# Kernel optimization log

Hardware: AMD Instinct MI355X
Metric: run time of the kernel (lower is better)

## Reference

```python
import jax, jax.numpy as jnp
import numpy as np

BN_EPS = 1e-5


def setup_inputs() -> dict:
    key = jax.random.key(0)
    ks = jax.random.split(key, 4)
    B, C, N = 4, 256, 4096
    Cq = C // 4
    return {
        "input_embedding": jax.random.normal(ks[0], (B, C, N), dtype=jnp.float32),
        "w_qk": jax.random.normal(ks[1], (Cq, C), dtype=jnp.float32) * (1.0 / np.sqrt(C)),
        "w_v": jax.random.normal(ks[2], (C, C), dtype=jnp.float32) * (1.0 / np.sqrt(C)),
        "b_v": jnp.zeros((C,), dtype=jnp.float32),
        "w_trans": jax.random.normal(ks[3], (C, C), dtype=jnp.float32) * (1.0 / np.sqrt(C)),
        "b_trans": jnp.zeros((C,), dtype=jnp.float32),
        "bn_gamma": jnp.ones((C,), dtype=jnp.float32),
        "bn_beta": jnp.zeros((C,), dtype=jnp.float32),
        "bn_mean": jnp.zeros((C,), dtype=jnp.float32),
        "bn_var": jnp.ones((C,), dtype=jnp.float32),
    }


def reference(input_embedding, w_qk, w_v, b_v, w_trans, b_trans,
              bn_gamma, bn_beta, bn_mean, bn_var):
    x = input_embedding  # (B, C, N)
    # 1x1 conv1d == channel matmul. Q and K share the same weight (tied in __init__).
    Q = jnp.einsum("qc,bcn->bnq", w_qk, x)              # (B, N, C/4)
    K = jnp.einsum("qc,bcn->bqn", w_qk, x)              # (B, C/4, N)
    V = jnp.einsum("oc,bcn->bon", w_v, x) + b_v[None, :, None]  # (B, C, N)
    scores = jnp.einsum("bnq,bqm->bnm", Q, K)           # (B, N, N)
    attn = jax.nn.softmax(scores, axis=-1)              # row softmax (dim=-1)
    # column L1 renormalization (sum over dim=1)
    attn = attn / (1e-9 + jnp.sum(attn, axis=1, keepdims=True))
    new_features = jnp.einsum("bcn,bnm->bcm", V, attn)  # (B, C, N)
    # offset residual -> trans conv -> BN (inference form) -> ReLU
    y = jnp.einsum("oc,bcn->bon", w_trans, x - new_features) + b_trans[None, :, None]
    inv_std = jax.lax.rsqrt(bn_var + BN_EPS)
    y = (y - bn_mean[None, :, None]) * (bn_gamma * inv_std)[None, :, None] + bn_beta[None, :, None]
    return jax.nn.relu(y)
```

## Files before the change

kernel.cpp:

```cpp
#include <hip/hip_runtime.h>

#define BATCH 4
#define CCH 256
#define NN 4096
#define CQ 64

typedef __bf16 bf16;
typedef __bf16 bf16x4 __attribute__((ext_vector_type(4)));
typedef __bf16 bf16x8 __attribute__((ext_vector_type(8)));
typedef float f32x4 __attribute__((ext_vector_type(4)));

static __device__ __forceinline__ f32x4 mfma16(bf16x8 a, bf16x8 b, f32x4 c) {
  return __builtin_amdgcn_mfma_f32_16x16x32_bf16(a, b, c, 0, 0, 0);
}

__global__ __launch_bounds__(256) void prep_kernel(const float* __restrict__ w_qk,
                                                   const float* __restrict__ w_v,
                                                   const float* __restrict__ w_trans,
                                                   bf16* __restrict__ wkvb,
                                                   bf16* __restrict__ wtb) {
  int i = blockIdx.x * 256 + threadIdx.x;
  if (i < 320 * 256) {
    int r = i >> 8, c = i & 255;
    float v = (r < 64) ? w_qk[r * 256 + c] : w_v[(r - 64) * 256 + c];
    wkvb[i] = (bf16)v;
  }
  if (i < 256 * 256) wtb[i] = (bf16)w_trans[i];
}

__global__ __launch_bounds__(256) void transpose_kernel(const float* __restrict__ x,
                                                        bf16* __restrict__ xTb) {
  __shared__ float t[64][65];
  int b = blockIdx.z, c0 = blockIdx.y * 64, n0 = blockIdx.x * 64;
  int tx = threadIdx.x & 63, ty = threadIdx.x >> 6;
  const float* xp = x + ((size_t)b * CCH + c0) * NN + n0;
#pragma unroll
  for (int j = 0; j < 16; ++j) {
    int cl = ty * 16 + j;
    t[tx][cl] = xp[(size_t)cl * NN + tx];
  }
  __syncthreads();
  bf16* op = xTb + ((size_t)b * NN + n0) * CCH + c0;
#pragma unroll
  for (int j = 0; j < 16; ++j) {
    int nl = ty * 16 + j;
    op[(size_t)nl * CCH + tx] = (bf16)t[nl][tx];
  }
}

__global__ __launch_bounds__(256) void kv_kernel(const bf16* __restrict__ wkvb,
                                                 const bf16* __restrict__ xTb,
                                                 const float* __restrict__ b_v,
                                                 bf16* __restrict__ Knq,
                                                 bf16* __restrict__ V,
                                                 float* __restrict__ sq) {
  int b = blockIdx.z, chunk = blockIdx.y;
  int w = threadIdx.x >> 6, lane = threadIdx.x & 63, lg = lane >> 4, lr = lane & 15;
  int n0 = blockIdx.x * 256 + w * 64;
  int r0 = chunk * 64;
  f32x4 z = {0.f, 0.f, 0.f, 0.f};
  f32x4 acc[4][4];
#pragma unroll
  for (int i = 0; i < 4; ++i)
#pragma unroll
    for (int j = 0; j < 4; ++j) acc[i][j] = z;

  for (int ks = 0; ks < 8; ++ks) {
    bf16x8 af[4], bb[4];
#pragma unroll
    for (int t = 0; t < 4; ++t)
      af[t] = *(const bf16x8*)(wkvb + (size_t)(r0 + 16 * t + lr) * 256 + 32 * ks + 8 * lg);
#pragma unroll
    for (int t = 0; t < 4; ++t)
      bb[t] = *(const bf16x8*)(xTb + ((size_t)b * NN + n0 + 16 * t + lr) * CCH + 32 * ks + 8 * lg);
#pragma unroll
    for (int tc = 0; tc < 4; ++tc)
#pragma unroll
      for (int tn = 0; tn < 4; ++tn) acc[tc][tn] = mfma16(af[tc], bb[tn], acc[tc][tn]);
  }

  if (chunk == 0) {
    float sqn[4];
#pragma unroll
    for (int tn = 0; tn < 4; ++tn) {
      int n = n0 + 16 * tn + lr;
#pragma unroll
      for (int tc = 0; tc < 4; ++tc) {
        bf16x4 kb;
#pragma unroll
        for (int r = 0; r < 4; ++r) kb[r] = (bf16)acc[tc][tn][r];
        *(bf16x4*)(Knq + ((size_t)b * NN + n) * CQ + 16 * tc + lg * 4) = kb;
      }
      float s = 0.f;
#pragma unroll
      for (int tc = 0; tc < 4; ++tc)
#pragma unroll
        for (int r = 0; r < 4; ++r) s += acc[tc][tn][r] * acc[tc][tn][r];
      s += __shfl_xor(s, 16);
      s += __shfl_xor(s, 32);
      sqn[tn] = s;
    }
    if (lane < 16) {
#pragma unroll
      for (int tn = 0; tn < 4; ++tn)
        sq[(size_t)b * NN + n0 + 16 * tn + lane] = sqn[tn];
    }
  } else {
#pragma unroll
    for (int tc = 0; tc < 4; ++tc) {
      int c4 = (chunk - 1) * 64 + 16 * tc + lg * 4;
      f32x4 bv = *(const f32x4*)(b_v + c4);
#pragma unroll
      for (int tn = 0; tn < 4; ++tn) {
        int n = n0 + 16 * tn + lr;
#pragma unroll
        for (int r = 0; r < 4; ++r)
          V[((size_t)b * CCH + c4 + r) * NN + n] = (bf16)(acc[tc][tn][r] + bv[r]);
      }
    }
  }
}

__global__ __launch_bounds__(512) void rnorm_kernel(const bf16* __restrict__ Knq,
                                                    const float* __restrict__ sq,
                                                    float* __restrict__ invr) {
  __shared__ float lsl[8][16];
  int b = blockIdx.y, n0 = blockIdx.x * 64;
  int w = threadIdx.x >> 6, lane = threadIdx.x & 63, lg = lane >> 4, lr = lane & 15;
  int sn = w & 3, mh = w >> 2;
  const bf16* Kb = Knq + (size_t)b * NN * CQ;
  int nr = n0 + 16 * sn;
  bf16x8 a0 = *(const bf16x8*)(Kb + (size_t)(nr + lr) * CQ + 8 * lg);
  bf16x8 a1 = *(const bf16x8*)(Kb + (size_t)(nr + lr) * CQ + 32 + 8 * lg);
  f32x4 sh = *(const f32x4*)(sq + (size_t)b * NN + nr + lg * 4);
  f32x4 z = {0.f, 0.f, 0.f, 0.f};
  f32x4 ls = z;
  for (int mt = mh * (NN / 2); mt < (mh + 1) * (NN / 2); mt += 64) {
#pragma unroll
    for (int j = 0; j < 4; ++j) {
      int m0 = mt + 16 * j;
      bf16x8 b0 = *(const bf16x8*)(Kb + (size_t)(m0 + lr) * CQ + 8 * lg);
      bf16x8 b1 = *(const bf16x8*)(Kb + (size_t)(m0 + lr) * CQ + 32 + 8 * lg);
      f32x4 s = mfma16(a0, b0, z);
      s = mfma16(a1, b1, s);
#pragma unroll
      for (int r = 0; r < 4; ++r) ls[r] += __expf(s[r] - sh[r]);
    }
  }
#pragma unroll
  for (int d = 1; d < 16; d <<= 1)
#pragma unroll
    for (int r = 0; r < 4; ++r) ls[r] += __shfl_xor(ls[r], d);
  if (lr == 0) {
#pragma unroll
    for (int r = 0; r < 4; ++r) lsl[w][lg * 4 + r] = ls[r];
  }
  __syncthreads();
  if (threadIdx.x < 64) {
    int t = threadIdx.x;
    float S = lsl[t >> 4][t & 15] + lsl[(t >> 4) + 4][t & 15];
    invr[(size_t)b * NN + n0 + t] = 1.0f / S;
  }
}

#define SWZ(row, colb) ((colb) ^ (((row)&7) << 4))
__global__ __launch_bounds__(512) void pv_kernel(const bf16* __restrict__ Knq,
                                                 const bf16* __restrict__ V,
                                                 const float* __restrict__ sq,
                                                 const float* __restrict__ invr,
                                                 const bf16* __restrict__ xTb,
                                                 bf16* __restrict__ DTb) {
  __shared__ bf16 P2[2][64][128];
  __shared__ float csl[8][64];
  __shared__ float csv[64];
  int lin = blockIdx.y * (NN / 64) + blockIdx.x;
  int xcd = lin & 7, slot = lin >> 3;
  int b = xcd >> 1;
  int m0 = (((xcd & 1) << 5) | slot) * 64;
  int w = threadIdx.x >> 6, lane = threadIdx.x & 63, lg = lane >> 4, lr = lane & 15;
  const bf16* Kb = Knq + (size_t)b * NN * CQ;
  const bf16* Vb = V + (size_t)b * CCH * NN;
  f32x4 z = {0.f, 0.f, 0.f, 0.f};

  bf16x8 bS[4][2];
#pragma unroll
  for (int tj = 0; tj < 4; ++tj) {
    bS[tj][0] = *(const bf16x8*)(Kb + (size_t)(m0 + 16 * tj + lr) * CQ + 8 * lg);
    bS[tj][1] = *(const bf16x8*)(Kb + (size_t)(m0 + 16 * tj + lr) * CQ + 32 + 8 * lg);
  }

  f32x4 acc[2][4];
#pragma unroll
  for (int i = 0; i < 2; ++i)
#pragma unroll
    for (int j = 0; j < 4; ++j) acc[i][j] = z;
  float cs[4] = {0.f, 0.f, 0.f, 0.f};

#define S_PHASE(STEP, BUF)                                                          \
  {                                                                                 \
    int nr_ = (STEP) * 128 + 16 * w;                                                \
    bf16x8 a0_ = *(const bf16x8*)(Kb + (size_t)(nr_ + lr) * CQ + 8 * lg);           \
    bf16x8 a1_ = *(const bf16x8*)(Kb + (size_t)(nr_ + lr) * CQ + 32 + 8 * lg);      \
    f32x4 sh_ = *(const f32x4*)(sq + (size_t)b * NN + nr_ + lg * 4);                \
    f32x4 ri_ = *(const f32x4*)(invr + (size_t)b * NN + nr_ + lg * 4);              \
    _Pragma("unroll") for (int tj = 0; tj < 4; ++tj) {                              \
      f32x4 s4 = mfma16(a0_, bS[tj][0], z);                                         \
      s4 = mfma16(a1_, bS[tj][1], s4);                                              \
      bf16x4 pb;                                                                    \
      _Pragma("unroll") for (int r = 0; r < 4; ++r) {                               \
        float p_ = __expf(s4[r] - sh_[r]) * ri_[r];                                 \
        cs[tj] += p_;                                                               \
        pb[r] = (bf16)p_;                                                           \
      }                                                                             \
      *(bf16x4*)((char*)&P2[BUF][16 * tj + lr][0] + SWZ(lr, 2 * (16 * w + 4 * lg))) = pb; \
    }                                                                               \
  }

  S_PHASE(0, 0);
  __syncthreads();

  for (int s = 0; s < NN / 128; ++s) {
    int cur = s & 1;
    int ns = s * 128;
    bf16x8 bp[4][4];
#pragma unroll
    for (int ks = 0; ks < 4; ++ks)
#pragma unroll
      for (int tj = 0; tj < 4; ++tj)
        bp[ks][tj] = *(const bf16x8*)((char*)&P2[cur][16 * tj + lr][0] +
                                      SWZ(16 * tj + lr, 2 * (32 * ks + 8 * lg)));
    bf16x8 av[4][2];
#pragma unroll
    for (int ks = 0; ks < 4; ++ks)
#pragma unroll
      for (int tc = 0; tc < 2; ++tc)
        av[ks][tc] = *(const bf16x8*)(Vb + (size_t)(32 * w + 16 * tc + lr) * NN + ns + 32 * ks + 8 * lg);
    if (s + 1 < NN / 128) S_PHASE(s + 1, cur ^ 1);
#pragma unroll
    for (int ks = 0; ks < 4; ++ks)
#pragma unroll
      for (int tc = 0; tc < 2; ++tc)
#pragma unroll
        for (int tj = 0; tj < 4; ++tj) acc[tc][tj] = mfma16(av[ks][tc], bp[ks][tj], acc[tc][tj]);
    __syncthreads();
  }

#pragma unroll
  for (int tj = 0; tj < 4; ++tj) {
    cs[tj] += __shfl_xor(cs[tj], 16);
    cs[tj] += __shfl_xor(cs[tj], 32);
  }
  if (lane < 16) {
#pragma unroll
    for (int tj = 0; tj < 4; ++tj) csl[w][16 * tj + lane] = cs[tj];
  }
  __syncthreads();
  if (threadIdx.x < 64) {
    int t = threadIdx.x;
    float s = 0.f;
#pragma unroll
    for (int ww = 0; ww < 8; ++ww) s += csl[ww][t];
    csv[t] = 1.0f / (1e-9f + s);
  }
  __syncthreads();

#pragma unroll
  for (int tj = 0; tj < 4; ++tj) {
    int ml = 16 * tj + lr;
    int m = m0 + ml;
    float ci = csv[ml];
#pragma unroll
    for (int tc = 0; tc < 2; ++tc) {
      int c4 = 32 * w + 16 * tc + lg * 4;
      bf16x4 xv = *(const bf16x4*)(xTb + ((size_t)b * NN + m) * CCH + c4);
      bf16x4 dv;
#pragma unroll
      for (int r = 0; r < 4; ++r) dv[r] = (bf16)((float)xv[r] - acc[tc][tj][r] * ci);
      *(bf16x4*)(DTb + ((size_t)b * NN + m) * CCH + c4) = dv;
    }
  }
}

__global__ __launch_bounds__(256) void final_kernel(const bf16* __restrict__ wtb,
                                                    const bf16* __restrict__ DTb,
                                                    const float* __restrict__ b_trans,
                                                    const float* __restrict__ gamma,
                                                    const float* __restrict__ beta,
                                                    const float* __restrict__ mean,
                                                    const float* __restrict__ var,
                                                    float* __restrict__ out) {
  int b = blockIdx.y;
  int w = threadIdx.x >> 6, lane = threadIdx.x & 63, lg = lane >> 4, lr = lane & 15;
  int n0 = blockIdx.x * 64;
  f32x4 z = {0.f, 0.f, 0.f, 0.f};
  f32x4 acc[4][4];
#pragma unroll
  for (int i = 0; i < 4; ++i)
#pragma unroll
    for (int j = 0; j < 4; ++j) acc[i][j] = z;

  for (int ks = 0; ks < 8; ++ks) {
    bf16x8 a[4], bb[4];
#pragma unroll
    for (int t = 0; t < 4; ++t)
      a[t] = *(const bf16x8*)(wtb + (size_t)(64 * w + 16 * t + lr) * 256 + 32 * ks + 8 * lg);
#pragma unroll
    for (int t = 0; t < 4; ++t)
      bb[t] = *(const bf16x8*)(DTb + ((size_t)b * NN + n0 + 16 * t + lr) * CCH + 32 * ks + 8 * lg);
#pragma unroll
    for (int tc = 0; tc < 4; ++tc)
#pragma unroll
      for (int tn = 0; tn < 4; ++tn) acc[tc][tn] = mfma16(a[tc], bb[tn], acc[tc][tn]);
  }

#pragma unroll
  for (int tc = 0; tc < 4; ++tc) {
    int c4 = 64 * w + 16 * tc + lg * 4;
    f32x4 bt = *(const f32x4*)(b_trans + c4);
    f32x4 gm = *(const f32x4*)(gamma + c4);
    f32x4 be = *(const f32x4*)(beta + c4);
    f32x4 mn = *(const f32x4*)(mean + c4);
    f32x4 vr = *(const f32x4*)(var + c4);
    f32x4 sc, shv;
#pragma unroll
    for (int r = 0; r < 4; ++r) {
      sc[r] = gm[r] * rsqrtf(vr[r] + 1e-5f);
      shv[r] = be[r] - mn[r] * sc[r];
    }
#pragma unroll
    for (int tn = 0; tn < 4; ++tn) {
      int n = n0 + 16 * tn + lr;
#pragma unroll
      for (int r = 0; r < 4; ++r) {
        float y = (acc[tc][tn][r] + bt[r]) * sc[r] + shv[r];
        out[((size_t)b * CCH + c4 + r) * NN + n] = fmaxf(y, 0.0f);
      }
    }
  }
}

extern "C" void kernel_launch(void* const* d_in, const int* in_sizes, int n_in,
                              void* d_out, int out_size, void* d_ws, size_t ws_size,
                              hipStream_t stream) {
  const float* x = (const float*)d_in[0];
  const float* w_qk = (const float*)d_in[1];
  const float* w_v = (const float*)d_in[2];
  const float* b_v = (const float*)d_in[3];
  const float* w_trans = (const float*)d_in[4];
  const float* b_trans = (const float*)d_in[5];
  const float* gamma = (const float*)d_in[6];
  const float* beta = (const float*)d_in[7];
  const float* mean = (const float*)d_in[8];
  const float* var = (const float*)d_in[9];
  float* out = (float*)d_out;

  char* p = (char*)d_ws;
  bf16* wkvb = (bf16*)p; p += (size_t)320 * 256 * 2;
  bf16* wtb = (bf16*)p;  p += (size_t)256 * 256 * 2;
  bf16* xTb = (bf16*)p;  p += (size_t)BATCH * NN * CCH * 2;
  bf16* Knq = (bf16*)p;  p += (size_t)BATCH * NN * CQ * 2;
  bf16* V = (bf16*)p;    p += (size_t)BATCH * CCH * NN * 2;
  float* sq = (float*)p;   p += (size_t)BATCH * NN * 4;
  float* invr = (float*)p; p += (size_t)BATCH * NN * 4;
  bf16* DTb = (bf16*)p;  p += (size_t)BATCH * NN * CCH * 2;

  hipLaunchKernelGGL(prep_kernel, dim3(320), dim3(256), 0, stream, w_qk, w_v, w_trans, wkvb, wtb);
  hipLaunchKernelGGL(transpose_kernel, dim3(NN / 64, CCH / 64, BATCH), dim3(256), 0, stream, x, xTb);
  hipLaunchKernelGGL(kv_kernel, dim3(NN / 256, 5, BATCH), dim3(256), 0, stream, wkvb, xTb, b_v, Knq, V, sq);
  hipLaunchKernelGGL(rnorm_kernel, dim3(NN / 64, BATCH), dim3(512), 0, stream, Knq, sq, invr);
  hipLaunchKernelGGL(pv_kernel, dim3(NN / 64, BATCH), dim3(512), 0, stream, Knq, V, sq, invr, xTb, DTb);
  hipLaunchKernelGGL(final_kernel, dim3(NN / 64, BATCH), dim3(256), 0, stream, wtb, DTb, b_trans, gamma, beta, mean, var, out);
}
```

Measured before the change: 287.6 us.

## Halve column tiles per block to double grid size across attention kernels

Every kernel now handles 32 columns per block instead of 64 (kv handles 128 instead of 256), so each launch has twice as many blocks. rnorm and pv drop from 512 to 256 threads with launch_bounds(256,2). Inside pv, each wave now owns 64 output channels and two 16-row score groups instead of 32 channels, which changes the work split and reuse inside the block. The aim is better CU occupancy and load balance on a wide GPU, at the cost of reading V from global memory twice as often per output column and doing more redundant K loads.

```diff
diff --git a/kernel.cpp b/kernel.cpp
--- a/kernel.cpp
+++ b/kernel.cpp
@@ -56,33 +56,34 @@
                                                  float* __restrict__ sq) {
   int b = blockIdx.z, chunk = blockIdx.y;
   int w = threadIdx.x >> 6, lane = threadIdx.x & 63, lg = lane >> 4, lr = lane & 15;
-  int n0 = blockIdx.x * 256 + w * 64;
+  int n0 = blockIdx.x * 128 + w * 32;
   int r0 = chunk * 64;
   f32x4 z = {0.f, 0.f, 0.f, 0.f};
-  f32x4 acc[4][4];
+  f32x4 acc[4][2];
 #pragma unroll
   for (int i = 0; i < 4; ++i)
 #pragma unroll
-    for (int j = 0; j < 4; ++j) acc[i][j] = z;
-
+    for (int j = 0; j < 2; ++j) acc[i][j] = z;
+
+#pragma unroll
   for (int ks = 0; ks < 8; ++ks) {
-    bf16x8 af[4], bb[4];
+    bf16x8 af[4], bb[2];
 #pragma unroll
     for (int t = 0; t < 4; ++t)
       af[t] = *(const bf16x8*)(wkvb + (size_t)(r0 + 16 * t + lr) * 256 + 32 * ks + 8 * lg);
 #pragma unroll
-    for (int t = 0; t < 4; ++t)
+    for (int t = 0; t < 2; ++t)
       bb[t] = *(const bf16x8*)(xTb + ((size_t)b * NN + n0 + 16 * t + lr) * CCH + 32 * ks + 8 * lg);
 #pragma unroll
     for (int tc = 0; tc < 4; ++tc)
 #pragma unroll
-      for (int tn = 0; tn < 4; ++tn) acc[tc][tn] = mfma16(af[tc], bb[tn], acc[tc][tn]);
+      for (int tn = 0; tn < 2; ++tn) acc[tc][tn] = mfma16(af[tc], bb[tn], acc[tc][tn]);
   }
 
   if (chunk == 0) {
-    float sqn[4];
-#pragma unroll
-    for (int tn = 0; tn < 4; ++tn) {
+    float sqn[2];
+#pragma unroll
+    for (int tn = 0; tn < 2; ++tn) {
       int n = n0 + 16 * tn + lr;
 #pragma unroll
       for (int tc = 0; tc < 4; ++tc) {
@@ -102,7 +103,7 @@
     }
     if (lane < 16) {
 #pragma unroll
-      for (int tn = 0; tn < 4; ++tn)
+      for (int tn = 0; tn < 2; ++tn)
         sq[(size_t)b * NN + n0 + 16 * tn + lane] = sqn[tn];
     }
   } else {
@@ -111,7 +112,7 @@
       int c4 = (chunk - 1) * 64 + 16 * tc + lg * 4;
       f32x4 bv = *(const f32x4*)(b_v + c4);
 #pragma unroll
-      for (int tn = 0; tn < 4; ++tn) {
+      for (int tn = 0; tn < 2; ++tn) {
         int n = n0 + 16 * tn + lr;
 #pragma unroll
         for (int r = 0; r < 4; ++r)
@@ -121,99 +122,113 @@
   }
 }
 
-__global__ __launch_bounds__(512) void rnorm_kernel(const bf16* __restrict__ Knq,
-                                                    const float* __restrict__ sq,
-                                                    float* __restrict__ invr) {
-  __shared__ float lsl[8][16];
-  int b = blockIdx.y, n0 = blockIdx.x * 64;
+__global__ __launch_bounds__(256, 2) void rnorm_kernel(const bf16* __restrict__ Knq,
+                                                       const float* __restrict__ sq,
+                                                       float* __restrict__ invr) {
+  __shared__ float lsl[4][2][16];
+  int b = blockIdx.y, n0 = blockIdx.x * 32;
   int w = threadIdx.x >> 6, lane = threadIdx.x & 63, lg = lane >> 4, lr = lane & 15;
-  int sn = w & 3, mh = w >> 2;
   const bf16* Kb = Knq + (size_t)b * NN * CQ;
-  int nr = n0 + 16 * sn;
-  bf16x8 a0 = *(const bf16x8*)(Kb + (size_t)(nr + lr) * CQ + 8 * lg);
-  bf16x8 a1 = *(const bf16x8*)(Kb + (size_t)(nr + lr) * CQ + 32 + 8 * lg);
-  f32x4 sh = *(const f32x4*)(sq + (size_t)b * NN + nr + lg * 4);
+  bf16x8 a0[2], a1[2];
+  f32x4 sh[2];
+#pragma unroll
+  for (int g = 0; g < 2; ++g) {
+    int nr = n0 + 16 * g;
+    a0[g] = *(const bf16x8*)(Kb + (size_t)(nr + lr) * CQ + 8 * lg);
+    a1[g] = *(const bf16x8*)(Kb + (size_t)(nr + lr) * CQ + 32 + 8 * lg);
+    sh[g] = *(const f32x4*)(sq + (size_t)b * NN + nr + lg * 4);
+  }
   f32x4 z = {0.f, 0.f, 0.f, 0.f};
-  f32x4 ls = z;
-  for (int mt = mh * (NN / 2); mt < (mh + 1) * (NN / 2); mt += 64) {
+  f32x4 ls[2] = {z, z};
+  for (int mt = w * (NN / 4); mt < (w + 1) * (NN / 4); mt += 64) {
 #pragma unroll
     for (int j = 0; j < 4; ++j) {
       int m0 = mt + 16 * j;
       bf16x8 b0 = *(const bf16x8*)(Kb + (size_t)(m0 + lr) * CQ + 8 * lg);
       bf16x8 b1 = *(const bf16x8*)(Kb + (size_t)(m0 + lr) * CQ + 32 + 8 * lg);
-      f32x4 s = mfma16(a0, b0, z);
-      s = mfma16(a1, b1, s);
-#pragma unroll
-      for (int r = 0; r < 4; ++r) ls[r] += __expf(s[r] - sh[r]);
+#pragma unroll
+      for (int g = 0; g < 2; ++g) {
+        f32x4 s = mfma16(a0[g], b0, z);
+        s = mfma16(a1[g], b1, s);
+#pragma unroll
+        for (int r = 0; r < 4; ++r) ls[g][r] += __expf(s[r] - sh[g][r]);
+      }
     }
   }
 #pragma unroll
   for (int d = 1; d < 16; d <<= 1)
 #pragma unroll
-    for (int r = 0; r < 4; ++r) ls[r] += __shfl_xor(ls[r], d);
+    for (int g = 0; g < 2; ++g)
+#pragma unroll
+      for (int r = 0; r < 4; ++r) ls[g][r] += __shfl_xor(ls[g][r], d);
   if (lr == 0) {
 #pragma unroll
-    for (int r = 0; r < 4; ++r) lsl[w][lg * 4 + r] = ls[r];
-  }
-  __syncthreads();
-  if (threadIdx.x < 64) {
-    int t = threadIdx.x;
-    float S = lsl[t >> 4][t & 15] + lsl[(t >> 4) + 4][t & 15];
-    invr[(size_t)b * NN + n0 + t] = 1.0f / S;
+    for (int g = 0; g < 2; ++g)
+#pragma unroll
+      for (int r = 0; r < 4; ++r) lsl[w][g][lg * 4 + r] = ls[g][r];
+  }
+  __syncthreads();
+  if (threadIdx.x < 32) {
+    int g = threadIdx.x >> 4, i = threadIdx.x & 15;
+    float S = lsl[0][g][i] + lsl[1][g][i] + lsl[2][g][i] + lsl[3][g][i];
+    invr[(size_t)b * NN + n0 + 16 * g + i] = 1.0f / S;
   }
 }
 
 #define SWZ(row, colb) ((colb) ^ (((row)&7) << 4))
-__global__ __launch_bounds__(512) void pv_kernel(const bf16* __restrict__ Knq,
-                                                 const bf16* __restrict__ V,
-                                                 const float* __restrict__ sq,
-                                                 const float* __restrict__ invr,
-                                                 const bf16* __restrict__ xTb,
-                                                 bf16* __restrict__ DTb) {
-  __shared__ bf16 P2[2][64][128];
-  __shared__ float csl[8][64];
-  __shared__ float csv[64];
-  int lin = blockIdx.y * (NN / 64) + blockIdx.x;
+__global__ __launch_bounds__(256, 2) void pv_kernel(const bf16* __restrict__ Knq,
+                                                    const bf16* __restrict__ V,
+                                                    const float* __restrict__ sq,
+                                                    const float* __restrict__ invr,
+                                                    const bf16* __restrict__ xTb,
+                                                    bf16* __restrict__ DTb) {
+  __shared__ bf16 P2[2][32][128];
+  __shared__ float csl[4][32];
+  __shared__ float csv[32];
+  int lin = blockIdx.y * (NN / 32) + blockIdx.x;
   int xcd = lin & 7, slot = lin >> 3;
   int b = xcd >> 1;
-  int m0 = (((xcd & 1) << 5) | slot) * 64;
+  int m0 = (((xcd & 1) << 6) | slot) * 32;
   int w = threadIdx.x >> 6, lane = threadIdx.x & 63, lg = lane >> 4, lr = lane & 15;
   const bf16* Kb = Knq + (size_t)b * NN * CQ;
   const bf16* Vb = V + (size_t)b * CCH * NN;
   f32x4 z = {0.f, 0.f, 0.f, 0.f};
 
-  bf16x8 bS[4][2];
-#pragma unroll
-  for (int tj = 0; tj < 4; ++tj) {
+  bf16x8 bS[2][2];
+#pragma unroll
+  for (int tj = 0; tj < 2; ++tj) {
     bS[tj][0] = *(const bf16x8*)(Kb + (size_t)(m0 + 16 * tj + lr) * CQ + 8 * lg);
     bS[tj][1] = *(const bf16x8*)(Kb + (size_t)(m0 + 16 * tj + lr) * CQ + 32 + 8 * lg);
   }
 
-  f32x4 acc[2][4];
-#pragma unroll
-  for (int i = 0; i < 2; ++i)
-#pragma unroll
-    for (int j = 0; j < 4; ++j) acc[i][j] = z;
-  float cs[4] = {0.f, 0.f, 0.f, 0.f};
-
-#define S_PHASE(STEP, BUF)                                                          \
-  {                                                                                 \
-    int nr_ = (STEP) * 128 + 16 * w;                                                \
-    bf16x8 a0_ = *(const bf16x8*)(Kb + (size_t)(nr_ + lr) * CQ + 8 * lg);           \
-    bf16x8 a1_ = *(const bf16x8*)(Kb + (size_t)(nr_ + lr) * CQ + 32 + 8 * lg);      \
-    f32x4 sh_ = *(const f32x4*)(sq + (size_t)b * NN + nr_ + lg * 4);                \
-    f32x4 ri_ = *(const f32x4*)(invr + (size_t)b * NN + nr_ + lg * 4);              \
-    _Pragma("unroll") for (int tj = 0; tj < 4; ++tj) {                              \
-      f32x4 s4 = mfma16(a0_, bS[tj][0], z);                                         \
-      s4 = mfma16(a1_, bS[tj][1], s4);                                              \
-      bf16x4 pb;                                                                    \
-      _Pragma("unroll") for (int r = 0; r < 4; ++r) {                               \
-        float p_ = __expf(s4[r] - sh_[r]) * ri_[r];                                 \
-        cs[tj] += p_;                                                               \
-        pb[r] = (bf16)p_;                                                           \
-      }                                                                             \
-      *(bf16x4*)((char*)&P2[BUF][16 * tj + lr][0] + SWZ(lr, 2 * (16 * w + 4 * lg))) = pb; \
-    }                                                                               \
+  f32x4 acc[4][2];
+#pragma unroll
+  for (int i = 0; i < 4; ++i)
+#pragma unroll
+    for (int j = 0; j < 2; ++j) acc[i][j] = z;
+  float cs[2] = {0.f, 0.f};
+
+#define S_PHASE(STEP, BUF)                                                            \
+  {                                                                                   \
+    _Pragma("unroll") for (int g = 0; g < 2; ++g) {                                   \
+      int nr_ = (STEP) * 128 + 32 * w + 16 * g;                                       \
+      bf16x8 a0_ = *(const bf16x8*)(Kb + (size_t)(nr_ + lr) * CQ + 8 * lg);           \
+      bf16x8 a1_ = *(const bf16x8*)(Kb + (size_t)(nr_ + lr) * CQ + 32 + 8 * lg);      \
+      f32x4 sh_ = *(const f32x4*)(sq + (size_t)b * NN + nr_ + lg * 4);                \
+      f32x4 ri_ = *(const f32x4*)(invr + (size_t)b * NN + nr_ + lg * 4);              \
+      _Pragma("unroll") for (int tj = 0; tj < 2; ++tj) {                              \
+        f32x4 s4 = mfma16(a0_, bS[tj][0], z);                                         \
+        s4 = mfma16(a1_, bS[tj][1], s4);                                              \
+        bf16x4 pb;                                                                    \
+        _Pragma("unroll") for (int r = 0; r < 4; ++r) {                               \
+          float p_ = __expf(s4[r] - sh_[r]) * ri_[r];                                 \
+          cs[tj] += p_;                                                               \
+          pb[r] = (bf16)p_;                                                           \
+        }                                                                             \
+        *(bf16x4*)((char*)&P2[BUF][16 * tj + lr][0] +                                 \
+                   SWZ(lr, 2 * (32 * w + 16 * g + 4 * lg))) = pb;                     \
+      }                                                                               \
+    }                                                                                 \
   }
 
   S_PHASE(0, 0);
@@ -222,56 +237,54 @@
   for (int s = 0; s < NN / 128; ++s) {
     int cur = s & 1;
     int ns = s * 128;
-    bf16x8 bp[4][4];
+    bf16x8 av[4][4];
 #pragma unroll
     for (int ks = 0; ks < 4; ++ks)
 #pragma unroll
-      for (int tj = 0; tj < 4; ++tj)
+      for (int tc = 0; tc < 4; ++tc)
+        av[ks][tc] = *(const bf16x8*)(Vb + (size_t)(64 * w + 16 * tc + lr) * NN + ns + 32 * ks + 8 * lg);
+    bf16x8 bp[4][2];
+#pragma unroll
+    for (int ks = 0; ks < 4; ++ks)
+#pragma unroll
+      for (int tj = 0; tj < 2; ++tj)
         bp[ks][tj] = *(const bf16x8*)((char*)&P2[cur][16 * tj + lr][0] +
                                       SWZ(16 * tj + lr, 2 * (32 * ks + 8 * lg)));
-    bf16x8 av[4][2];
+    if (s + 1 < NN / 128) S_PHASE(s + 1, cur ^ 1);
 #pragma unroll
     for (int ks = 0; ks < 4; ++ks)
 #pragma unroll
-      for (int tc = 0; tc < 2; ++tc)
-        av[ks][tc] = *(const bf16x8*)(Vb + (size_t)(32 * w + 16 * tc + lr) * NN + ns + 32 * ks + 8 * lg);
-    if (s + 1 < NN / 128) S_PHASE(s + 1, cur ^ 1);
-#pragma unroll
-    for (int ks = 0; ks < 4; ++ks)
-#pragma unroll
-      for (int tc = 0; tc < 2; ++tc)
-#pragma unroll
-        for (int tj = 0; tj < 4; ++tj) acc[tc][tj] = mfma16(av[ks][tc], bp[ks][tj], acc[tc][tj]);
+      for (int tc = 0; tc < 4; ++tc)
+#pragma unroll
+        for (int tj = 0; tj < 2; ++tj) acc[tc][tj] = mfma16(av[ks][tc], bp[ks][tj], acc[tc][tj]);
     __syncthreads();
   }
 
 #pragma unroll
-  for (int tj = 0; tj < 4; ++tj) {
+  for (int tj = 0; tj < 2; ++tj) {
     cs[tj] += __shfl_xor(cs[tj], 16);
     cs[tj] += __shfl_xor(cs[tj], 32);
   }
   if (lane < 16) {
 #pragma unroll
-    for (int tj = 0; tj < 4; ++tj) csl[w][16 * tj + lane] = cs[tj];
-  }
-  __syncthreads();
-  if (threadIdx.x < 64) {
+    for (int tj = 0; tj < 2; ++tj) csl[w][16 * tj + lane] = cs[tj];
+  }
+  __syncthreads();
+  if (threadIdx.x < 32) {
     int t = threadIdx.x;
-    float s = 0.f;
-#pragma unroll
-    for (int ww = 0; ww < 8; ++ww) s += csl[ww][t];
+    float s = csl[0][t] + csl[1][t] + csl[2][t] + csl[3][t];
     csv[t] = 1.0f / (1e-9f + s);
   }
   __syncthreads();
 
 #pragma unroll
-  for (int tj = 0; tj < 4; ++tj) {
+  for (int tj = 0; tj < 2; ++tj) {
     int ml = 16 * tj + lr;
     int m = m0 + ml;
     float ci = csv[ml];
 #pragma unroll
-    for (int tc = 0; tc < 2; ++tc) {
-      int c4 = 32 * w + 16 * tc + lg * 4;
+    for (int tc = 0; tc < 4; ++tc) {
+      int c4 = 64 * w + 16 * tc + lg * 4;
       bf16x4 xv = *(const bf16x4*)(xTb + ((size_t)b * NN + m) * CCH + c4);
       bf16x4 dv;
 #pragma unroll
@@ -291,26 +304,27 @@
                                                     float* __restrict__ out) {
   int b = blockIdx.y;
   int w = threadIdx.x >> 6, lane = threadIdx.x & 63, lg = lane >> 4, lr = lane & 15;
-  int n0 = blockIdx.x * 64;
+  int n0 = blockIdx.x * 32;
   f32x4 z = {0.f, 0.f, 0.f, 0.f};
-  f32x4 acc[4][4];
+  f32x4 acc[4][2];
 #pragma unroll
   for (int i = 0; i < 4; ++i)
 #pragma unroll
-    for (int j = 0; j < 4; ++j) acc[i][j] = z;
-
+    for (int j = 0; j < 2; ++j) acc[i][j] = z;
+
+#pragma unroll
   for (int ks = 0; ks < 8; ++ks) {
-    bf16x8 a[4], bb[4];
+    bf16x8 a[4], bb[2];
 #pragma unroll
     for (int t = 0; t < 4; ++t)
       a[t] = *(const bf16x8*)(wtb + (size_t)(64 * w + 16 * t + lr) * 256 + 32 * ks + 8 * lg);
 #pragma unroll
-    for (int t = 0; t < 4; ++t)
+    for (int t = 0; t < 2; ++t)
       bb[t] = *(const bf16x8*)(DTb + ((size_t)b * NN + n0 + 16 * t + lr) * CCH + 32 * ks + 8 * lg);
 #pragma unroll
     for (int tc = 0; tc < 4; ++tc)
 #pragma unroll
-      for (int tn = 0; tn < 4; ++tn) acc[tc][tn] = mfma16(a[tc], bb[tn], acc[tc][tn]);
+      for (int tn = 0; tn < 2; ++tn) acc[tc][tn] = mfma16(a[tc], bb[tn], acc[tc][tn]);
   }
 
 #pragma unroll
@@ -328,7 +342,7 @@
       shv[r] = be[r] - mn[r] * sc[r];
     }
 #pragma unroll
-    for (int tn = 0; tn < 4; ++tn) {
+    for (int tn = 0; tn < 2; ++tn) {
       int n = n0 + 16 * tn + lr;
 #pragma unroll
       for (int r = 0; r < 4; ++r) {
@@ -366,8 +380,8 @@
 
   hipLaunchKernelGGL(prep_kernel, dim3(320), dim3(256), 0, stream, w_qk, w_v, w_trans, wkvb, wtb);
   hipLaunchKernelGGL(transpose_kernel, dim3(NN / 64, CCH / 64, BATCH), dim3(256), 0, stream, x, xTb);
-  hipLaunchKernelGGL(kv_kernel, dim3(NN / 256, 5, BATCH), dim3(256), 0, stream, wkvb, xTb, b_v, Knq, V, sq);
-  hipLaunchKernelGGL(rnorm_kernel, dim3(NN / 64, BATCH), dim3(512), 0, stream, Knq, sq, invr);
-  hipLaunchKernelGGL(pv_kernel, dim3(NN / 64, BATCH), dim3(512), 0, stream, Knq, V, sq, invr, xTb, DTb);
-  hipLaunchKernelGGL(final_kernel, dim3(NN / 64, BATCH), dim3(256), 0, stream, wtb, DTb, b_trans, gamma, beta, mean, var, out);
-}
+  hipLaunchKernelGGL(kv_kernel, dim3(NN / 128, 5, BATCH), dim3(256), 0, stream, wkvb, xTb, b_v, Knq, V, sq);
+  hipLaunchKernelGGL(rnorm_kernel, dim3(NN / 32, BATCH), dim3(256), 0, stream, Knq, sq, invr);
+  hipLaunchKernelGGL(pv_kernel, dim3(NN / 32, BATCH), dim3(256), 0, stream, Knq, V, sq, invr, xTb, DTb);
+  hipLaunchKernelGGL(final_kernel, dim3(NN / 32, BATCH), dim3(256), 0, stream, wtb, DTb, b_trans, gamma, beta, mean, var, out);
+}
```

New measurement: 348.8 us. 21.3% more time.

## Split attention-PV work across channel halves and shrink tiles for more blocks

Applied to the files above, without the earlier changes.

The PV kernel now launches 512 blocks of 256 threads, each handling half the channels (128) for a 64-column tile. Each wave computes two 16-row score groups so that four waves cover the 128-row window, with a wider LDS swizzle. The V loads are also issued before the LDS P reads. Separately, kv and final kernels use narrower N tiles to double the block count, and rnorm drops its two-way split and shared-memory reduction. The goal is better occupancy and CU fill. The cost is that the score/exp work is recomputed twice per column tile, once per channel half.

```diff
diff --git a/kernel.cpp b/kernel.cpp
--- a/kernel.cpp
+++ b/kernel.cpp
@@ -56,33 +56,34 @@
                                                  float* __restrict__ sq) {
   int b = blockIdx.z, chunk = blockIdx.y;
   int w = threadIdx.x >> 6, lane = threadIdx.x & 63, lg = lane >> 4, lr = lane & 15;
-  int n0 = blockIdx.x * 256 + w * 64;
+  int n0 = blockIdx.x * 128 + w * 32;
   int r0 = chunk * 64;
   f32x4 z = {0.f, 0.f, 0.f, 0.f};
-  f32x4 acc[4][4];
+  f32x4 acc[4][2];
 #pragma unroll
   for (int i = 0; i < 4; ++i)
 #pragma unroll
-    for (int j = 0; j < 4; ++j) acc[i][j] = z;
-
+    for (int j = 0; j < 2; ++j) acc[i][j] = z;
+
+#pragma unroll
   for (int ks = 0; ks < 8; ++ks) {
-    bf16x8 af[4], bb[4];
+    bf16x8 af[4], bb[2];
 #pragma unroll
     for (int t = 0; t < 4; ++t)
       af[t] = *(const bf16x8*)(wkvb + (size_t)(r0 + 16 * t + lr) * 256 + 32 * ks + 8 * lg);
 #pragma unroll
-    for (int t = 0; t < 4; ++t)
+    for (int t = 0; t < 2; ++t)
       bb[t] = *(const bf16x8*)(xTb + ((size_t)b * NN + n0 + 16 * t + lr) * CCH + 32 * ks + 8 * lg);
 #pragma unroll
     for (int tc = 0; tc < 4; ++tc)
 #pragma unroll
-      for (int tn = 0; tn < 4; ++tn) acc[tc][tn] = mfma16(af[tc], bb[tn], acc[tc][tn]);
+      for (int tn = 0; tn < 2; ++tn) acc[tc][tn] = mfma16(af[tc], bb[tn], acc[tc][tn]);
   }
 
   if (chunk == 0) {
-    float sqn[4];
-#pragma unroll
-    for (int tn = 0; tn < 4; ++tn) {
+    float sqn[2];
+#pragma unroll
+    for (int tn = 0; tn < 2; ++tn) {
       int n = n0 + 16 * tn + lr;
 #pragma unroll
       for (int tc = 0; tc < 4; ++tc) {
@@ -102,7 +103,7 @@
     }
     if (lane < 16) {
 #pragma unroll
-      for (int tn = 0; tn < 4; ++tn)
+      for (int tn = 0; tn < 2; ++tn)
         sq[(size_t)b * NN + n0 + 16 * tn + lane] = sqn[tn];
     }
   } else {
@@ -111,7 +112,7 @@
       int c4 = (chunk - 1) * 64 + 16 * tc + lg * 4;
       f32x4 bv = *(const f32x4*)(b_v + c4);
 #pragma unroll
-      for (int tn = 0; tn < 4; ++tn) {
+      for (int tn = 0; tn < 2; ++tn) {
         int n = n0 + 16 * tn + lr;
 #pragma unroll
         for (int r = 0; r < 4; ++r)
@@ -121,21 +122,19 @@
   }
 }
 
-__global__ __launch_bounds__(512) void rnorm_kernel(const bf16* __restrict__ Knq,
+__global__ __launch_bounds__(256) void rnorm_kernel(const bf16* __restrict__ Knq,
                                                     const float* __restrict__ sq,
                                                     float* __restrict__ invr) {
-  __shared__ float lsl[8][16];
   int b = blockIdx.y, n0 = blockIdx.x * 64;
   int w = threadIdx.x >> 6, lane = threadIdx.x & 63, lg = lane >> 4, lr = lane & 15;
-  int sn = w & 3, mh = w >> 2;
   const bf16* Kb = Knq + (size_t)b * NN * CQ;
-  int nr = n0 + 16 * sn;
+  int nr = n0 + 16 * w;
   bf16x8 a0 = *(const bf16x8*)(Kb + (size_t)(nr + lr) * CQ + 8 * lg);
   bf16x8 a1 = *(const bf16x8*)(Kb + (size_t)(nr + lr) * CQ + 32 + 8 * lg);
   f32x4 sh = *(const f32x4*)(sq + (size_t)b * NN + nr + lg * 4);
   f32x4 z = {0.f, 0.f, 0.f, 0.f};
   f32x4 ls = z;
-  for (int mt = mh * (NN / 2); mt < (mh + 1) * (NN / 2); mt += 64) {
+  for (int mt = 0; mt < NN; mt += 64) {
 #pragma unroll
     for (int j = 0; j < 4; ++j) {
       int m0 = mt + 16 * j;
@@ -153,30 +152,26 @@
     for (int r = 0; r < 4; ++r) ls[r] += __shfl_xor(ls[r], d);
   if (lr == 0) {
 #pragma unroll
-    for (int r = 0; r < 4; ++r) lsl[w][lg * 4 + r] = ls[r];
-  }
-  __syncthreads();
-  if (threadIdx.x < 64) {
-    int t = threadIdx.x;
-    float S = lsl[t >> 4][t & 15] + lsl[(t >> 4) + 4][t & 15];
-    invr[(size_t)b * NN + n0 + t] = 1.0f / S;
-  }
-}
-
-#define SWZ(row, colb) ((colb) ^ (((row)&7) << 4))
-__global__ __launch_bounds__(512) void pv_kernel(const bf16* __restrict__ Knq,
-                                                 const bf16* __restrict__ V,
-                                                 const float* __restrict__ sq,
-                                                 const float* __restrict__ invr,
-                                                 const bf16* __restrict__ xTb,
-                                                 bf16* __restrict__ DTb) {
+    for (int r = 0; r < 4; ++r)
+      invr[(size_t)b * NN + nr + lg * 4 + r] = 1.0f / ls[r];
+  }
+}
+
+#define SWZ5(row, colb) ((colb) ^ (((row)&7) << 5))
+__global__ __launch_bounds__(256, 2) void pv_kernel(const bf16* __restrict__ Knq,
+                                                    const bf16* __restrict__ V,
+                                                    const float* __restrict__ sq,
+                                                    const float* __restrict__ invr,
+                                                    const bf16* __restrict__ xTb,
+                                                    bf16* __restrict__ DTb) {
   __shared__ bf16 P2[2][64][128];
-  __shared__ float csl[8][64];
+  __shared__ float csl[4][64];
   __shared__ float csv[64];
-  int lin = blockIdx.y * (NN / 64) + blockIdx.x;
+  int lin = blockIdx.x;
   int xcd = lin & 7, slot = lin >> 3;
   int b = xcd >> 1;
-  int m0 = (((xcd & 1) << 5) | slot) * 64;
+  int m0 = (((xcd & 1) << 5) | (slot & 31)) * 64;
+  int c0 = (slot >> 5) * 128;
   int w = threadIdx.x >> 6, lane = threadIdx.x & 63, lg = lane >> 4, lr = lane & 15;
   const bf16* Kb = Knq + (size_t)b * NN * CQ;
   const bf16* Vb = V + (size_t)b * CCH * NN;
@@ -196,24 +191,27 @@
     for (int j = 0; j < 4; ++j) acc[i][j] = z;
   float cs[4] = {0.f, 0.f, 0.f, 0.f};
 
-#define S_PHASE(STEP, BUF)                                                          \
-  {                                                                                 \
-    int nr_ = (STEP) * 128 + 16 * w;                                                \
-    bf16x8 a0_ = *(const bf16x8*)(Kb + (size_t)(nr_ + lr) * CQ + 8 * lg);           \
-    bf16x8 a1_ = *(const bf16x8*)(Kb + (size_t)(nr_ + lr) * CQ + 32 + 8 * lg);      \
-    f32x4 sh_ = *(const f32x4*)(sq + (size_t)b * NN + nr_ + lg * 4);                \
-    f32x4 ri_ = *(const f32x4*)(invr + (size_t)b * NN + nr_ + lg * 4);              \
-    _Pragma("unroll") for (int tj = 0; tj < 4; ++tj) {                              \
-      f32x4 s4 = mfma16(a0_, bS[tj][0], z);                                         \
-      s4 = mfma16(a1_, bS[tj][1], s4);                                              \
-      bf16x4 pb;                                                                    \
-      _Pragma("unroll") for (int r = 0; r < 4; ++r) {                               \
-        float p_ = __expf(s4[r] - sh_[r]) * ri_[r];                                 \
-        cs[tj] += p_;                                                               \
-        pb[r] = (bf16)p_;                                                           \
-      }                                                                             \
-      *(bf16x4*)((char*)&P2[BUF][16 * tj + lr][0] + SWZ(lr, 2 * (16 * w + 4 * lg))) = pb; \
-    }                                                                               \
+#define S_PHASE(WIN, BUF)                                                              \
+  {                                                                                    \
+    _Pragma("unroll") for (int g = 0; g < 2; ++g) {                                    \
+      int nrb = (WIN) * 128 + 32 * w + 16 * g;                                         \
+      bf16x8 k0_ = *(const bf16x8*)(Kb + (size_t)(nrb + lr) * CQ + 8 * lg);            \
+      bf16x8 k1_ = *(const bf16x8*)(Kb + (size_t)(nrb + lr) * CQ + 32 + 8 * lg);       \
+      f32x4 sh_ = *(const f32x4*)(sq + (size_t)b * NN + nrb + lg * 4);                 \
+      f32x4 ri_ = *(const f32x4*)(invr + (size_t)b * NN + nrb + lg * 4);               \
+      _Pragma("unroll") for (int tj = 0; tj < 4; ++tj) {                               \
+        f32x4 s4 = mfma16(k0_, bS[tj][0], z);                                          \
+        s4 = mfma16(k1_, bS[tj][1], s4);                                               \
+        bf16x4 pb;                                                                     \
+        _Pragma("unroll") for (int r = 0; r < 4; ++r) {                                \
+          float p_ = __expf(s4[r] - sh_[r]) * ri_[r];                                  \
+          cs[tj] += p_;                                                                \
+          pb[r] = (bf16)p_;                                                            \
+        }                                                                              \
+        *(bf16x4*)((char*)&P2[BUF][16 * tj + lr][0] +                                  \
+                   SWZ5(lr, 2 * (32 * w + 16 * g + 4 * lg))) = pb;                     \
+      }                                                                                \
+    }                                                                                  \
   }
 
   S_PHASE(0, 0);
@@ -222,19 +220,20 @@
   for (int s = 0; s < NN / 128; ++s) {
     int cur = s & 1;
     int ns = s * 128;
+    bf16x8 av[4][2];
+#pragma unroll
+    for (int ks = 0; ks < 4; ++ks)
+#pragma unroll
+      for (int tc = 0; tc < 2; ++tc)
+        av[ks][tc] = *(const bf16x8*)(Vb + (size_t)(c0 + 32 * w + 16 * tc + lr) * NN +
+                                      ns + 32 * ks + 8 * lg);
     bf16x8 bp[4][4];
 #pragma unroll
     for (int ks = 0; ks < 4; ++ks)
 #pragma unroll
       for (int tj = 0; tj < 4; ++tj)
         bp[ks][tj] = *(const bf16x8*)((char*)&P2[cur][16 * tj + lr][0] +
-                                      SWZ(16 * tj + lr, 2 * (32 * ks + 8 * lg)));
-    bf16x8 av[4][2];
-#pragma unroll
-    for (int ks = 0; ks < 4; ++ks)
-#pragma unroll
-      for (int tc = 0; tc < 2; ++tc)
-        av[ks][tc] = *(const bf16x8*)(Vb + (size_t)(32 * w + 16 * tc + lr) * NN + ns + 32 * ks + 8 * lg);
+                                      SWZ5(16 * tj + lr, 2 * (32 * ks + 8 * lg)));
     if (s + 1 < NN / 128) S_PHASE(s + 1, cur ^ 1);
 #pragma unroll
     for (int ks = 0; ks < 4; ++ks)
@@ -257,9 +256,7 @@
   __syncthreads();
   if (threadIdx.x < 64) {
     int t = threadIdx.x;
-    float s = 0.f;
-#pragma unroll
-    for (int ww = 0; ww < 8; ++ww) s += csl[ww][t];
+    float s = csl[0][t] + csl[1][t] + csl[2][t] + csl[3][t];
     csv[t] = 1.0f / (1e-9f + s);
   }
   __syncthreads();
@@ -271,7 +268,7 @@
     float ci = csv[ml];
 #pragma unroll
     for (int tc = 0; tc < 2; ++tc) {
-      int c4 = 32 * w + 16 * tc + lg * 4;
+      int c4 = c0 + 32 * w + 16 * tc + 4 * lg;
       bf16x4 xv = *(const bf16x4*)(xTb + ((size_t)b * NN + m) * CCH + c4);
       bf16x4 dv;
 #pragma unroll
@@ -291,26 +288,27 @@
                                                     float* __restrict__ out) {
   int b = blockIdx.y;
   int w = threadIdx.x >> 6, lane = threadIdx.x & 63, lg = lane >> 4, lr = lane & 15;
-  int n0 = blockIdx.x * 64;
+  int n0 = blockIdx.x * 32;
   f32x4 z = {0.f, 0.f, 0.f, 0.f};
-  f32x4 acc[4][4];
+  f32x4 acc[4][2];
 #pragma unroll
   for (int i = 0; i < 4; ++i)
 #pragma unroll
-    for (int j = 0; j < 4; ++j) acc[i][j] = z;
-
+    for (int j = 0; j < 2; ++j) acc[i][j] = z;
+
+#pragma unroll
   for (int ks = 0; ks < 8; ++ks) {
-    bf16x8 a[4], bb[4];
+    bf16x8 a[4], bb[2];
 #pragma unroll
     for (int t = 0; t < 4; ++t)
       a[t] = *(const bf16x8*)(wtb + (size_t)(64 * w + 16 * t + lr) * 256 + 32 * ks + 8 * lg);
 #pragma unroll
-    for (int t = 0; t < 4; ++t)
+    for (int t = 0; t < 2; ++t)
       bb[t] = *(const bf16x8*)(DTb + ((size_t)b * NN + n0 + 16 * t + lr) * CCH + 32 * ks + 8 * lg);
 #pragma unroll
     for (int tc = 0; tc < 4; ++tc)
 #pragma unroll
-      for (int tn = 0; tn < 4; ++tn) acc[tc][tn] = mfma16(a[tc], bb[tn], acc[tc][tn]);
+      for (int tn = 0; tn < 2; ++tn) acc[tc][tn] = mfma16(a[tc], bb[tn], acc[tc][tn]);
   }
 
 #pragma unroll
@@ -328,7 +326,7 @@
       shv[r] = be[r] - mn[r] * sc[r];
     }
 #pragma unroll
-    for (int tn = 0; tn < 4; ++tn) {
+    for (int tn = 0; tn < 2; ++tn) {
       int n = n0 + 16 * tn + lr;
 #pragma unroll
       for (int r = 0; r < 4; ++r) {
@@ -366,8 +364,8 @@
 
   hipLaunchKernelGGL(prep_kernel, dim3(320), dim3(256), 0, stream, w_qk, w_v, w_trans, wkvb, wtb);
   hipLaunchKernelGGL(transpose_kernel, dim3(NN / 64, CCH / 64, BATCH), dim3(256), 0, stream, x, xTb);
-  hipLaunchKernelGGL(kv_kernel, dim3(NN / 256, 5, BATCH), dim3(256), 0, stream, wkvb, xTb, b_v, Knq, V, sq);
-  hipLaunchKernelGGL(rnorm_kernel, dim3(NN / 64, BATCH), dim3(512), 0, stream, Knq, sq, invr);
-  hipLaunchKernelGGL(pv_kernel, dim3(NN / 64, BATCH), dim3(512), 0, stream, Knq, V, sq, invr, xTb, DTb);
-  hipLaunchKernelGGL(final_kernel, dim3(NN / 64, BATCH), dim3(256), 0, stream, wtb, DTb, b_trans, gamma, beta, mean, var, out);
-}
+  hipLaunchKernelGGL(kv_kernel, dim3(NN / 128, 5, BATCH), dim3(256), 0, stream, wkvb, xTb, b_v, Knq, V, sq);
+  hipLaunchKernelGGL(rnorm_kernel, dim3(NN / 64, BATCH), dim3(256), 0, stream, Knq, sq, invr);
+  hipLaunchKernelGGL(pv_kernel, dim3(512), dim3(256), 0, stream, Knq, V, sq, invr, xTb, DTb);
+  hipLaunchKernelGGL(final_kernel, dim3(NN / 32, BATCH), dim3(256), 0, stream, wtb, DTb, b_trans, gamma, beta, mean, var, out);
+}
```

Result: slower. 297.1 us (+3.3%).
